# Kernel optimization log

Hardware: AMD Instinct MI355X
Metric: run time of the kernel (lower is better)

The kernel has to match this reference:

```python
import jax, jax.numpy as jnp
import numpy as np

N, S, D, d, H = 8, 2048, 256, 128, 10  # H = rel_k_heights
SCALING = float(np.sqrt(2 * d))


def _ln(x, g, b):
    m = jnp.mean(x, axis=-1, keepdims=True)
    v = jnp.var(x, axis=-1, keepdims=True)
    return (x - m) / jnp.sqrt(v + 1e-5) * g + b


def setup_inputs() -> dict:
    key = jax.random.key(0)
    ks = jax.random.split(key, 12)
    std = 0.02
    p = lambda k, shape: (jax.random.normal(k, shape, jnp.float32) * std)
    return {
        'sequence': jax.random.normal(ks[0], (N, S, D), jnp.float32),
        'attention_mask': jax.random.bernoulli(ks[1], 0.9, (N, S, S)),
        'heights': jax.random.randint(ks[2], (N, S), 0, 50),
        'W_init': p(ks[3], (D, D)), 'b_init': jnp.zeros((D,), jnp.float32),
        'ln_g': jnp.ones((D,), jnp.float32), 'ln_b': jnp.zeros((D,), jnp.float32),
        'W_U': p(ks[4], (D, 2 * D)), 'b_U': jnp.zeros((2 * D,), jnp.float32),
        'W_V': p(ks[5], (D, 2 * D)), 'b_V': jnp.zeros((2 * D,), jnp.float32),
        'W_Z': p(ks[6], (D, d)), 'b_Z': jnp.zeros((d,), jnp.float32),
        'os_gamma': p(ks[7], (3, d)),  # torch inits gamma ~ N(0, 0.02)
        'os_beta': jnp.zeros((3, d), jnp.float32),
        'embed_heights': jax.random.normal(ks[8], (H, d), jnp.float32),
        'W_out': p(ks[9], (2 * D, D)), 'b_out': jnp.zeros((D,), jnp.float32),
        'W_gate': p(ks[10], (2 * D, D)), 'b_gate': jnp.zeros((D,), jnp.float32),
    }


def reference(sequence, attention_mask, heights,
              W_init, b_init, ln_g, ln_b,
              W_U, b_U, W_V, b_V, W_Z, b_Z,
              os_gamma, os_beta, embed_heights,
              W_out, b_out, W_gate, b_gate):
    S0 = (S - 1) // 2  # 1023
    mask = attention_mask[:, :S0, S0:]          # [N,S0,S1]
    res = sequence

    x = _ln(sequence @ W_init + b_init, ln_g, ln_b)            # [N,S,D]
    U = jax.nn.silu(x[:, :S0, :] @ W_U + b_U)                  # [N,S0,2D]
    Z = jax.nn.silu(x @ W_Z + b_Z)                             # [N,S,d]
    V = jax.nn.silu(x[:, S0:, :] @ W_V + b_V)                  # [N,S1,2D]

    # OffsetScale: Q, Qp, K from Z
    Q = (Z * os_gamma[0] + os_beta[0])[:, :S0, :]              # [N,S0,d]
    Qp = (Z * os_gamma[1] + os_beta[1])[:, :S0, :]             # [N,S0,d]
    K = (Z * os_gamma[2] + os_beta[2])[:, S0:, :]              # [N,S1,d]

    energy = jnp.einsum('bsd,btd->bst', Q, K)                  # [N,S0,S1]

    # relative-height bias: direct gather (math-equivalent to one-hot*sum)
    Q_h = jnp.einsum('bsd,hd->bsh', Qp, embed_heights)         # [N,S0,H]
    rel = heights[:, None, S0:] - heights[:, :S0, None]        # [N,S0,S1]
    rel_idx = jnp.clip(rel, 1, H) - 1
    rel_energy = jnp.take_along_axis(Q_h, rel_idx, axis=2)     # [N,S0,S1]

    logits = (energy + rel_energy) / SCALING
    logits = jnp.where(mask, logits, -9999.0)
    attn = jax.nn.softmax(logits, axis=-1)                     # [N,S0,S1]

    V_ = jnp.einsum('bst,btd->bsd', attn, V)                   # [N,S0,2D]
    out = (U * V_) @ W_out + b_out                             # [N,S0,D]
    gates = jax.nn.sigmoid(
        jnp.concatenate([out, res[:, :S0, :]], axis=-1) @ W_gate + b_gate)
    out = gates * out + (1.0 - gates) * res[:, :S0, :]
    out = jnp.concatenate([out, res[:, S0:, :]], axis=1)       # [N,S,D]
    return out
```

## Files before the change

### kernel.cpp

```cpp
#include <hip/hip_runtime.h>
#include <cstdint>
#include <cstddef>

#define S_TOT 2048
#define S0_   1023
#define S1_   1025
#define D_    256
#define D2_   512
#define DZ_   128
#define NB_   8
#define NT_   17
#define KT16_ 68
#define SCALE_INV (1.0f/16.0f)
#define XPAD  264
#define UPAD  520
#define NTILES (NB_*S0_*NT_)
#define MP_BLOCKS ((NTILES + 15)/16)

typedef __attribute__((ext_vector_type(8))) short short8v;
typedef __attribute__((ext_vector_type(4))) short short4v;
typedef __attribute__((ext_vector_type(4))) float f32x4;
typedef unsigned long long u64;

__device__ __forceinline__ short f2bf(float f){
  unsigned u = __float_as_uint(f);
  unsigned r = (u + 0x7FFFu + ((u >> 16) & 1u)) >> 16;
  return (short)r;
}
__device__ __forceinline__ float bf2f(short s){
  return __uint_as_float(((unsigned)(unsigned short)s) << 16);
}
__device__ __forceinline__ float silu_f(float x){ return x / (1.f + __expf(-x)); }

__device__ __forceinline__ short8v load_afrag(const short* arow, int kt, int khi){
  short4v lo = *reinterpret_cast<const short4v*>(arow + kt*32 + khi);
  short4v hi = *reinterpret_cast<const short4v*>(arow + kt*32 + khi + 16);
  short8v r = {lo[0],lo[1],lo[2],lo[3],hi[0],hi[1],hi[2],hi[3]};
  return r;
}

__global__ __launch_bounds__(256) void k_prep(
    const float* __restrict__ W_init, const float* __restrict__ W_U,
    const float* __restrict__ W_V,    const float* __restrict__ W_Z,
    const float* __restrict__ W_out,  const float* __restrict__ W_gate,
    short* __restrict__ WpI, short* __restrict__ WpU, short* __restrict__ WpV,
    short* __restrict__ WpZ, short* __restrict__ WpO, short* __restrict__ WpG,
    const unsigned char* __restrict__ amask, u64* __restrict__ maskb)
{
  const int blk = blockIdx.x;
  if (blk < 304){
    const float* W; short* dst; int K, N, base;
    if      (blk <  32){ W=W_init; dst=WpI; K=256; N=256; base=0;   }
    else if (blk <  96){ W=W_U;    dst=WpU; K=256; N=512; base=32;  }
    else if (blk < 160){ W=W_V;    dst=WpV; K=256; N=512; base=96;  }
    else if (blk < 176){ W=W_Z;    dst=WpZ; K=256; N=128; base=160; }
    else if (blk < 240){ W=W_out;  dst=WpO; K=512; N=256; base=176; }
    else               { W=W_gate; dst=WpG; K=512; N=256; base=240; }
    const int wv = threadIdx.x >> 6, lane = threadIdx.x & 63;
    const int KT = K >> 5;
    const int tile = (blk - base)*4 + wv;
    const int nt = tile / KT, kt = tile - nt*KT;
    const int n = nt*16 + (lane & 15);
    const int kbase = kt*32 + ((lane>>4)<<2);
    short8v v;
    #pragma unroll
    for (int j=0;j<8;++j){
      int k = kbase + (j&3) + ((j>>2)<<4);
      v[j] = f2bf(W[(size_t)k*N + n]);
    }
    *reinterpret_cast<short8v*>(dst + ((size_t)tile*64 + lane)*8) = v;
  } else {
    const int lane = threadIdx.x & 63;
    const int g0 = ((blk - 304)*4 + (threadIdx.x >> 6))*4;
    #pragma unroll
    for (int j=0;j<4;++j){
      int tg = g0 + j;
      if (tg >= NTILES) break;
      int row = tg / NT_;
      int t   = tg - row*NT_;
      int b   = row / S0_;
      int q   = row - b*S0_;
      int key = t*64 + lane;
      unsigned char v = 0;
      if (key < S1_) v = amask[((size_t)(b*S_TOT + q))*S_TOT + S0_ + key];
      u64 bits = __ballot(v != 0);
      if (lane == 0) maskb[tg] = bits;
    }
  }
}

__global__ __launch_bounds__(256) void k_x(
    const float* __restrict__ seq, const short* __restrict__ Wp,
    const float* __restrict__ b_init,
    const float* __restrict__ ln_g, const float* __restrict__ ln_b,
    short* __restrict__ xb, float* __restrict__ out)
{
  __shared__ short s_a[64*XPAD];
  const int tid = threadIdx.x, lane = tid & 63, wv = tid >> 6;
  const int R0 = blockIdx.x * 64;
  const int colb = lane & 15, khi = (lane>>4)<<2;

  for (int c = tid; c < 64*64; c += 256){
    int row = c >> 6, c4 = (c & 63) << 2;
    int g = R0 + row;
    float4 f = *reinterpret_cast<const float4*>(seq + (size_t)g*D_ + c4);
    short4v h = { f2bf(f.x), f2bf(f.y), f2bf(f.z), f2bf(f.w) };
    *reinterpret_cast<short4v*>(&s_a[row*XPAD + c4]) = h;
    if ((g & 2047) >= S0_)
      *reinterpret_cast<float4*>(out + (size_t)g*D_ + c4) = f;
  }
  __syncthreads();

  f32x4 acc[16];
  #pragma unroll
  for (int nt=0;nt<16;++nt) acc[nt] = (f32x4){0.f,0.f,0.f,0.f};

  const short* arow = &s_a[(wv*16 + colb)*XPAD];
  #pragma unroll
  for (int kt=0; kt<8; ++kt){
    short8v a = load_afrag(arow, kt, khi);
    #pragma unroll
    for (int nt=0; nt<16; ++nt){
      short8v b = *reinterpret_cast<const short8v*>(Wp + ((size_t)(nt*8 + kt)*64 + lane)*8);
      acc[nt] = __builtin_amdgcn_mfma_f32_16x16x32_bf16(a, b, acc[nt], 0, 0, 0);
    }
  }

  float sum[4] = {0.f,0.f,0.f,0.f};
  #pragma unroll
  for (int nt=0; nt<16; ++nt){
    float bv = b_init[nt*16 + colb];
    #pragma unroll
    for (int r=0;r<4;++r){ acc[nt][r] += bv; sum[r] += acc[nt][r]; }
  }
  #pragma unroll
  for (int r=0;r<4;++r){
    #pragma unroll
    for (int m=1;m<16;m<<=1) sum[r] += __shfl_xor(sum[r], m, 64);
    sum[r] *= (1.f/256.f);
  }
  float var[4] = {0.f,0.f,0.f,0.f};
  #pragma unroll
  for (int nt=0; nt<16; ++nt)
    #pragma unroll
    for (int r=0;r<4;++r){ float d = acc[nt][r]-sum[r]; var[r] += d*d; }
  #pragma unroll
  for (int r=0;r<4;++r){
    #pragma unroll
    for (int m=1;m<16;m<<=1) var[r] += __shfl_xor(var[r], m, 64);
    var[r] = rsqrtf(var[r]*(1.f/256.f) + 1e-5f);
  }
  #pragma unroll
  for (int nt=0; nt<16; ++nt){
    int col = nt*16 + colb;
    float g = ln_g[col], bb = ln_b[col];
    #pragma unroll
    for (int r=0;r<4;++r){
      float xn = (acc[nt][r]-sum[r])*var[r]*g + bb;
      s_a[(wv*16 + ((lane>>4)<<2) + r)*XPAD + col] = f2bf(xn);
    }
  }
  __syncthreads();
  for (int c = tid; c < 64*32; c += 256){
    int row = c >> 5, c8 = (c & 31) << 3;
    *reinterpret_cast<short8v*>(xb + (size_t)(R0+row)*D_ + c8) =
        *reinterpret_cast<const short8v*>(&s_a[row*XPAD + c8]);
  }
}

__global__ __launch_bounds__(256) void k_gemmZV(
    const short* __restrict__ xb,
    const short* __restrict__ WpZ, const float* __restrict__ b_Z,
    short* __restrict__ Zb, short* __restrict__ ZkF,
    const short* __restrict__ WpV, const float* __restrict__ b_V,
    short* __restrict__ VtF)
{
  __shared__ short s_a[64*XPAD];
  __shared__ short s_t[64][72];
  const int blk = blockIdx.x;
  const int tid = threadIdx.x, lane = tid & 63, wv = tid >> 6;
  const int wy = wv >> 1, wx = wv & 1;
  const int colb = lane & 15, khi = (lane>>4)<<2;

  if (blk < 512){
    const int R0 = (blk >> 1) * 64;
    const int C0 = (blk & 1) * 64;

    for (int c = tid; c < 64*32; c += 256){
      int r = c >> 5, c8 = (c & 31) << 3;
      size_t xrow = (size_t)(R0 + r);
      *reinterpret_cast<short8v*>(&s_a[r*XPAD + c8]) =
          *reinterpret_cast<const short8v*>(xb + xrow*D_ + c8);
    }
    __syncthreads();

    f32x4 acc[2][2];
    #pragma unroll
    for(int i=0;i<2;++i)
      #pragma unroll
      for(int j=0;j<2;++j) acc[i][j] = (f32x4){0.f,0.f,0.f,0.f};

    const short* ar0 = &s_a[(wy*32 + colb)*XPAD];
    const short* ar1 = ar0 + 16*XPAD;
    const int ntg = (C0 >> 4) + wx*2;
    #pragma unroll
    for (int kt=0; kt<8; ++kt){
      short8v a0 = load_afrag(ar0, kt, khi);
      short8v a1 = load_afrag(ar1, kt, khi);
      short8v b0 = *reinterpret_cast<const short8v*>(WpZ + ((size_t)((ntg+0)*8 + kt)*64 + lane)*8);
      short8v b1 = *reinterpret_cast<const short8v*>(WpZ + ((size_t)((ntg+1)*8 + kt)*64 + lane)*8);
      acc[0][0] = __builtin_amdgcn_mfma_f32_16x16x32_bf16(a0, b0, acc[0][0], 0,0,0);
      acc[0][1] = __builtin_amdgcn_mfma_f32_16x16x32_bf16(a0, b1, acc[0][1], 0,0,0);
      acc[1][0] = __builtin_amdgcn_mfma_f32_16x16x32_bf16(a1, b0, acc[1][0], 0,0,0);
      acc[1][1] = __builtin_amdgcn_mfma_f32_16x16x32_bf16(a1, b1, acc[1][1], 0,0,0);
    }
    #pragma unroll
    for (int sj=0; sj<2; ++sj){
      int cl = wx*32 + sj*16 + colb;
      int col = C0 + cl;
      float bv = b_Z[col];
      #pragma unroll
      for (int si=0; si<2; ++si){
        #pragma unroll
        for (int r=0;r<4;++r){
          int rl = wy*32 + si*16 + ((lane>>4)<<2) + r;
          short zv = f2bf(silu_f(acc[si][sj][r] + bv));
          Zb[(size_t)(R0 + rl)*DZ_ + col] = zv;
          s_t[rl][cl] = zv;
        }
      }
    }
    __syncthreads();
    {
      const int r  = tid >> 2, hi = tid & 3;
      const int g  = R0 + r;
      const int s  = g & 2047;
      const int bb2= g >> 11;
      const int k  = s - S0_;
      if (k >= 0 && k <= 1024){
        const int kt16 = k >> 4, lcol = k & 15;
        const int lane2 = hi*16 + lcol;
        #pragma unroll
        for (int ktl=0; ktl<2; ++ktl){
          const int ktg = (C0 >> 5) + ktl;
          short8v f;
          #pragma unroll
          for (int j=0;j<8;++j){
            int dzl = ktl*32 + hi*4 + (j&3) + ((j>>2)<<4);
            f[j] = s_t[r][dzl];
          }
          size_t o = (((size_t)(bb2*KT16_ + kt16)*4 + ktg)*64 + lane2);
          *reinterpret_cast<short8v*>(ZkF + o*8) = f;
        }
      }
    }
  } else {
    const int idx = blk - 512;
    const int t   = idx % 17;
    const int rest= idx / 17;
    const int C0  = (rest & 7) * 64;
    const int b   = rest >> 3;
    const int R0  = t * 64;

    for (int c = tid; c < 64*32; c += 256){
      int r = c >> 5, c8 = (c & 31) << 3;
      int k = R0 + r; if (k > 1024) k = 1024;
      size_t xrow = (size_t)b*S_TOT + S0_ + k;
      *reinterpret_cast<short8v*>(&s_a[r*XPAD + c8]) =
          *reinterpret_cast<const short8v*>(xb + xrow*D_ + c8);
    }
    __syncthreads();

    f32x4 acc[2][2];
    #pragma unroll
    for(int i=0;i<2;++i)
      #pragma unroll
      for(int j=0;j<2;++j) acc[i][j] = (f32x4){0.f,0.f,0.f,0.f};

    const short* ar0 = &s_a[(wy*32 + colb)*XPAD];
    const short* ar1 = ar0 + 16*XPAD;
    const int ntg = (C0 >> 4) + wx*2;
    #pragma unroll
    for (int kt=0; kt<8; ++kt){
      short8v a0 = load_afrag(ar0, kt, khi);
      short8v a1 = load_afrag(ar1, kt, khi);
      short8v b0 = *reinterpret_cast<const short8v*>(WpV + ((size_t)((ntg+0)*8 + kt)*64 + lane)*8);
      short8v b1 = *reinterpret_cast<const short8v*>(WpV + ((size_t)((ntg+1)*8 + kt)*64 + lane)*8);
      acc[0][0] = __builtin_amdgcn_mfma_f32_16x16x32_bf16(a0, b0, acc[0][0], 0,0,0);
      acc[0][1] = __builtin_amdgcn_mfma_f32_16x16x32_bf16(a0, b1, acc[0][1], 0,0,0);
      acc[1][0] = __builtin_amdgcn_mfma_f32_16x16x32_bf16(a1, b0, acc[1][0], 0,0,0);
      acc[1][1] = __builtin_amdgcn_mfma_f32_16x16x32_bf16(a1, b1, acc[1][1], 0,0,0);
    }
    #pragma unroll
    for (int sj=0; sj<2; ++sj){
      int cl = wx*32 + sj*16 + colb;
      float bv = b_V[C0 + cl];
      #pragma unroll
      for (int si=0; si<2; ++si){
        #pragma unroll
        for (int r=0;r<4;++r){
          int rl = wy*32 + si*16 + ((lane>>4)<<2) + r;
          s_t[cl][rl] = f2bf(silu_f(acc[si][sj][r] + bv));
        }
      }
    }
    __syncthreads();
    {
      const int vt_l = tid >> 6;
      const int vloc = vt_l*16 + (lane & 15);
      const int krow = (lane>>4)<<2;
      #pragma unroll
      for (int kt=0; kt<2; ++kt){
        short8v f;
        #pragma unroll
        for (int j=0;j<8;++j){
          int kl = kt*32 + krow + (j&3) + ((j>>2)<<4);
          short v = s_t[vloc][kl];
          if (R0 + kl >= S1_) v = 0;
          f[j] = v;
        }
        size_t o = (((size_t)b*32 + (C0>>4) + vt_l)*(2*NT_) + 2*t + kt)*64 + lane;
        *reinterpret_cast<short8v*>(VtF + o*8) = f;
      }
    }
  }
}

#define SMEM_BYTES 103424
__global__ __launch_bounds__(512,2) void k_flash(
    const short* __restrict__ Zb, const short* __restrict__ ZkF,
    const short* __restrict__ VtF, const u64* __restrict__ maskb,
    const short* __restrict__ xb,
    const short* __restrict__ WpU, const float* __restrict__ b_U,
    const short* __restrict__ Wpo, const float* __restrict__ b_out,
    const short* __restrict__ Wpg, const float* __restrict__ b_gate,
    const float* __restrict__ seq, float* __restrict__ out,
    const int* __restrict__ heights,
    const float* __restrict__ os_g, const float* __restrict__ os_b,
    const float* __restrict__ embH)
{
  __shared__ __align__(16) char smem[SMEM_BYTES];
  __shared__ float  s_qh[32][12];
  __shared__ float  s_qb[32];
  __shared__ int    s_hk[NT_*64];
  __shared__ u64    s_mb[32][NT_];
  __shared__ float  s_mxA[8][16], s_mxB[8][16];
  __shared__ float  s_smA[8][16], s_smB[8][16];

  short8v (*s_pAl)[64] = reinterpret_cast<short8v(*)[64]>(smem);
  short8v (*s_pAh)[64] = reinterpret_cast<short8v(*)[64]>(smem + 17408);
  short8v (*s_pBl)[64] = reinterpret_cast<short8v(*)[64]>(smem + 34816);
  short8v (*s_pBh)[64] = reinterpret_cast<short8v(*)[64]>(smem + 52224);
  short   (*s_qg)[132] = reinterpret_cast<short(*)[132]>(smem + 34816);
  short* sUV = reinterpret_cast<short*>(smem);
  short* sO  = reinterpret_cast<short*>(smem + 34816);
  short* sX  = reinterpret_cast<short*>(smem + 69632);
  short* sR  = reinterpret_cast<short*>(smem + 86528);

  const int tid = threadIdx.x, lane = tid & 63, wv = tid >> 6;
  const int b  = blockIdx.x & 7;
  const int qp = blockIdx.x >> 3;
  const int q0 = qp * 32;

  for (int c = tid; c < 32*32; c += 512){
    int r = c >> 5, c8 = (c & 31) << 3;
    int q = min(q0 + r, S0_-1);
    *reinterpret_cast<short8v*>(&sX[r*XPAD + c8]) =
        *reinterpret_cast<const short8v*>(xb + ((size_t)(b*S_TOT + q))*D_ + c8);
  }
  for (int c = tid; c < 32*64; c += 512){
    int r = c >> 6, c4 = (c & 63) << 2;
    int q = min(q0 + r, S0_-1);
    float4 f = *reinterpret_cast<const float4*>(seq + ((size_t)(b*S_TOT + q))*D_ + c4);
    short4v h = { f2bf(f.x), f2bf(f.y), f2bf(f.z), f2bf(f.w) };
    *reinterpret_cast<short4v*>(&sR[r*XPAD + c4]) = h;
  }

  {
    int row = tid >> 4, part = tid & 15;
    int q = q0 + row; if (q > S0_-1) q = S0_-1;
    const short* zrow = Zb + ((size_t)(b*S_TOT + q))*DZ_ + part*8;
    float qb_acc = 0.f;
    float qh_acc[10];
    #pragma unroll
    for (int h=0;h<10;++h) qh_acc[h] = 0.f;
    #pragma unroll
    for (int e=0; e<8; ++e){
      int dz = part*8 + e;
      float z = bf2f(zrow[e]);
      float Q  = z*os_g[dz]      + os_b[dz];
      float Qp = z*os_g[DZ_+dz]  + os_b[DZ_+dz];
      s_qg[row][dz] = f2bf(Q * os_g[2*DZ_+dz]);
      qb_acc += Q * os_b[2*DZ_+dz];
      #pragma unroll
      for (int h=0;h<10;++h) qh_acc[h] += Qp * embH[h*DZ_ + dz];
    }
    #pragma unroll
    for (int m=1;m<16;m<<=1){
      qb_acc += __shfl_xor(qb_acc, m, 64);
      #pragma unroll
      for (int h=0;h<10;++h) qh_acc[h] += __shfl_xor(qh_acc[h], m, 64);
    }
    if (part == 0){
      s_qb[row] = qb_acc;
      #pragma unroll
      for (int h=0;h<10;++h) s_qh[row][h] = qh_acc[h];
    }
  }
  for (int k = tid; k < NT_*64; k += 512)
    s_hk[k] = (k < S1_) ? heights[b*S_TOT + S0_ + k] : 0;
  for (int idx = tid; idx < 32*NT_; idx += 512){
    int qq = idx / NT_, tt = idx - qq*NT_;
    int qr = min(q0 + qq, S0_-1);
    s_mb[qq][tt] = maskb[((size_t)(b*S0_ + qr))*NT_ + tt];
  }
  __syncthreads();

  const int qcol = lane & 15, khi = (lane>>4)<<2;
  const int hqA = heights[b*S_TOT + min(q0 + qcol,      S0_-1)];
  const int hqB = heights[b*S_TOT + min(q0 + 16 + qcol, S0_-1)];
  const float qbA = s_qb[qcol], qbB = s_qb[16 + qcol];

  short8v qgfA[4], qgfB[4];
  #pragma unroll
  for (int kt=0; kt<4; ++kt){
    qgfA[kt] = load_afrag(&s_qg[qcol][0],      kt, khi);
    qgfB[kt] = load_afrag(&s_qg[16 + qcol][0], kt, khi);
  }

  f32x4 scA[3][4], scB[3][4];
  float tmA = -1e30f, tmB = -1e30f;
  #pragma unroll
  for (int it=0; it<3; ++it){
    const int t = it*8 + wv;
    if (t < NT_){
      u64 mbA = s_mb[qcol][t], mbB = s_mb[16 + qcol][t];
      #pragma unroll
      for (int st=0; st<4; ++st){
        f32x4 cA = (f32x4){0.f,0.f,0.f,0.f};
        f32x4 cB = (f32x4){0.f,0.f,0.f,0.f};
        #pragma unroll
        for (int kt=0; kt<4; ++kt){
          short8v a = *reinterpret_cast<const short8v*>(
              ZkF + (((size_t)(b*KT16_ + t*4 + st)*4 + kt)*64 + lane)*8);
          cA = __builtin_amdgcn_mfma_f32_16x16x32_bf16(a, qgfA[kt], cA, 0,0,0);
          cB = __builtin_amdgcn_mfma_f32_16x16x32_bf16(a, qgfB[kt], cB, 0,0,0);
        }
        int4 hk4 = *reinterpret_cast<const int4*>(&s_hk[t*64 + st*16 + khi]);
        #pragma unroll
        for (int r=0;r<4;++r){
          int hk = (&hk4.x)[r];
          int kl = st*16 + khi + r;
          int iA = min(max(hk - hqA, 1), 10) - 1;
          float vA = (cA[r] + qbA + s_qh[qcol][iA]) * SCALE_INV;
          vA = ((mbA >> kl) & 1ull) ? vA : -9999.f;
          cA[r] = vA; tmA = fmaxf(tmA, vA);
          int iB = min(max(hk - hqB, 1), 10) - 1;
          float vB = (cB[r] + qbB + s_qh[16 + qcol][iB]) * SCALE_INV;
          vB = ((mbB >> kl) & 1ull) ? vB : -9999.f;
          cB[r] = vB; tmB = fmaxf(tmB, vB);
        }
        scA[it][st] = cA; scB[it][st] = cB;
      }
    }
  }
  tmA = fmaxf(tmA, __shfl_xor(tmA, 16, 64));
  tmA = fmaxf(tmA, __shfl_xor(tmA, 32, 64));
  tmB = fmaxf(tmB, __shfl_xor(tmB, 16, 64));
  tmB = fmaxf(tmB, __shfl_xor(tmB, 32, 64));
  if (lane < 16){ s_mxA[wv][lane] = tmA; s_mxB[wv][lane] = tmB; }
  __syncthreads();

  float mA = -1e30f, mB = -1e30f;
  #pragma unroll
  for (int w=0; w<8; ++w){
    mA = fmaxf(mA, s_mxA[w][qcol]);
    mB = fmaxf(mB, s_mxB[w][qcol]);
  }
  float lsA = 0.f, lsB = 0.f;
  #pragma unroll
  for (int it=0; it<3; ++it){
    const int t = it*8 + wv;
    if (t < NT_){
      #pragma unroll
      for (int st=0; st<4; ++st)
        #pragma unroll
        for (int r=0;r<4;++r){
          float pA = __expf(scA[it][st][r] - mA); lsA += pA; scA[it][st][r] = pA;
          float pB = __expf(scB[it][st][r] - mB); lsB += pB; scB[it][st][r] = pB;
        }
      short8v a0, a1, b0, b1;
      #pragma unroll
      for (int j=0;j<8;++j){
        a0[j] = f2bf(scA[it][(j>>2)][j&3]);
        a1[j] = f2bf(scA[it][2 + (j>>2)][j&3]);
        b0[j] = f2bf(scB[it][(j>>2)][j&3]);
        b1[j] = f2bf(scB[it][2 + (j>>2)][j&3]);
      }
      s_pAl[t][lane] = a0; s_pAh[t][lane] = a1;
      s_pBl[t][lane] = b0; s_pBh[t][lane] = b1;
    }
  }
  lsA += __shfl_xor(lsA, 16, 64); lsA += __shfl_xor(lsA, 32, 64);
  lsB += __shfl_xor(lsB, 16, 64); lsB += __shfl_xor(lsB, 32, 64);
  if (lane < 16){ s_smA[wv][lane] = lsA; s_smB[wv][lane] = lsB; }
  __syncthreads();

  float lrA[4], lrB[4];
  #pragma unroll
  for (int r=0;r<4;++r){
    int qr = khi + r;
    float sa = 0.f, sb = 0.f;
    #pragma unroll
    for (int w=0; w<8; ++w){ sa += s_smA[w][qr]; sb += s_smB[w][qr]; }
    lrA[r] = sa; lrB[r] = sb;
  }
  f32x4 OA[4], OB[4];
  #pragma unroll
  for (int j=0;j<4;++j){ OA[j] = (f32x4){0.f,0.f,0.f,0.f}; OB[j] = (f32x4){0.f,0.f,0.f,0.f}; }
  for (int t=0; t<NT_; ++t){
    short8v pa0 = s_pAl[t][lane], pa1 = s_pAh[t][lane];
    short8v pb0 = s_pBl[t][lane], pb1 = s_pBh[t][lane];
    #pragma unroll
    for (int j=0;j<4;++j){
      size_t vb = ((size_t)b*32 + wv*4 + j)*(2*NT_) + 2*t;
      short8v v0 = *reinterpret_cast<const short8v*>(VtF + (vb*64 + lane)*8);
      short8v v1 = *reinterpret_cast<const short8v*>(VtF + ((vb+1)*64 + lane)*8);
      OA[j] = __builtin_amdgcn_mfma_f32_16x16x32_bf16(pa0, v0, OA[j], 0,0,0);
      OA[j] = __builtin_amdgcn_mfma_f32_16x16x32_bf16(pa1, v1, OA[j], 0,0,0);
      OB[j] = __builtin_amdgcn_mfma_f32_16x16x32_bf16(pb0, v0, OB[j], 0,0,0);
      OB[j] = __builtin_amdgcn_mfma_f32_16x16x32_bf16(pb1, v1, OB[j], 0,0,0);
    }
  }
  __syncthreads();

  f32x4 auA[4], auB[4];
  #pragma unroll
  for (int j=0;j<4;++j){ auA[j] = (f32x4){0.f,0.f,0.f,0.f}; auB[j] = (f32x4){0.f,0.f,0.f,0.f}; }
  {
    const short* xrA = &sX[qcol*XPAD];
    const short* xrB = &sX[(16 + qcol)*XPAD];
    #pragma unroll
    for (int kt=0; kt<8; ++kt){
      short8v aA = load_afrag(xrA, kt, khi);
      short8v aB = load_afrag(xrB, kt, khi);
      #pragma unroll
      for (int j=0;j<4;++j){
        int nt = wv*4 + j;
        short8v bw = *reinterpret_cast<const short8v*>(WpU + ((size_t)(nt*8 + kt)*64 + lane)*8);
        auA[j] = __builtin_amdgcn_mfma_f32_16x16x32_bf16(aA, bw, auA[j], 0,0,0);
        auB[j] = __builtin_amdgcn_mfma_f32_16x16x32_bf16(aB, bw, auB[j], 0,0,0);
      }
    }
  }
  float invA[4], invB[4];
  #pragma unroll
  for (int r=0;r<4;++r){ invA[r] = 1.f / lrA[r]; invB[r] = 1.f / lrB[r]; }
  #pragma unroll
  for (int j=0;j<4;++j){
    int v = wv*64 + j*16 + qcol;
    float bu = b_U[v];
    #pragma unroll
    for (int r=0;r<4;++r){
      float uA = silu_f(auA[j][r] + bu);
      sUV[(khi + r)*UPAD + v] = f2bf(uA * OA[j][r] * invA[r]);
      float uB = silu_f(auB[j][r] + bu);
      sUV[(16 + khi + r)*UPAD + v] = f2bf(uB * OB[j][r] * invB[r]);
    }
  }
  __syncthreads();

  f32x4 aoA[2], aoB[2];
  #pragma unroll
  for (int j=0;j<2;++j){ aoA[j] = (f32x4){0.f,0.f,0.f,0.f}; aoB[j] = (f32x4){0.f,0.f,0.f,0.f}; }
  {
    const short* uvA = &sUV[qcol*UPAD];
    const short* uvB = &sUV[(16 + qcol)*UPAD];
    #pragma unroll
    for (int kt=0; kt<16; ++kt){
      short8v aA = load_afrag(uvA, kt, khi);
      short8v aB = load_afrag(uvB, kt, khi);
      #pragma unroll
      for (int j=0;j<2;++j){
        int nt = wv*2 + j;
        short8v bw = *reinterpret_cast<const short8v*>(Wpo + ((size_t)(nt*16 + kt)*64 + lane)*8);
        aoA[j] = __builtin_amdgcn_mfma_f32_16x16x32_bf16(aA, bw, aoA[j], 0,0,0);
        aoB[j] = __builtin_amdgcn_mfma_f32_16x16x32_bf16(aB, bw, aoB[j], 0,0,0);
      }
    }
  }
  #pragma unroll
  for (int j=0;j<2;++j){
    int col = (wv*2+j)*16 + qcol;
    float bv = b_out[col];
    #pragma unroll
    for (int r=0;r<4;++r){
      aoA[j][r] += bv;  sO[(khi + r)*XPAD + col]      = f2bf(aoA[j][r]);
      aoB[j][r] += bv;  sO[(16 + khi + r)*XPAD + col] = f2bf(aoB[j][r]);
    }
  }
  __syncthreads();

  f32x4 agA[2], agB[2];
  #pragma unroll
  for (int j=0;j<2;++j){ agA[j] = (f32x4){0.f,0.f,0.f,0.f}; agB[j] = (f32x4){0.f,0.f,0.f,0.f}; }
  {
    const short* oA = &sO[qcol*XPAD];
    const short* oB = &sO[(16 + qcol)*XPAD];
    const short* rA = &sR[qcol*XPAD];
    const short* rB = &sR[(16 + qcol)*XPAD];
    #pragma unroll
    for (int kt=0; kt<8; ++kt){
      short8v aA = load_afrag(oA, kt, khi);
      short8v aB = load_afrag(oB, kt, khi);
      #pragma unroll
      for (int j=0;j<2;++j){
        int nt = wv*2 + j;
        short8v bw = *reinterpret_cast<const short8v*>(Wpg + ((size_t)(nt*16 + kt)*64 + lane)*8);
        agA[j] = __builtin_amdgcn_mfma_f32_16x16x32_bf16(aA, bw, agA[j], 0,0,0);
        agB[j] = __builtin_amdgcn_mfma_f32_16x16x32_bf16(aB, bw, agB[j], 0,0,0);
      }
    }
    #pragma unroll
    for (int kt=0; kt<8; ++kt){
      short8v aA = load_afrag(rA, kt, khi);
      short8v aB = load_afrag(rB, kt, khi);
      #pragma unroll
      for (int j=0;j<2;++j){
        int nt = wv*2 + j;
        short8v bw = *reinterpret_cast<const short8v*>(Wpg + ((size_t)(nt*16 + 8 + kt)*64 + lane)*8);
        agA[j] = __builtin_amdgcn_mfma_f32_16x16x32_bf16(aA, bw, agA[j], 0,0,0);
        agB[j] = __builtin_amdgcn_mfma_f32_16x16x32_bf16(aB, bw, agB[j], 0,0,0);
      }
    }
  }
  #pragma unroll
  for (int j=0;j<2;++j){
    int col = (wv*2+j)*16 + qcol;
    float bg = b_gate[col];
    #pragma unroll
    for (int r=0;r<4;++r){
      int qA = q0 + khi + r;
      if (qA < S0_){
        float res = seq[((size_t)(b*S_TOT + qA))*D_ + col];
        float g = 1.f/(1.f + __expf(-(agA[j][r] + bg)));
        out[((size_t)(b*S_TOT + qA))*D_ + col] = g*aoA[j][r] + (1.f-g)*res;
      }
      int qB = q0 + 16 + khi + r;
      if (qB < S0_){
        float res = seq[((size_t)(b*S_TOT + qB))*D_ + col];
        float g = 1.f/(1.f + __expf(-(agB[j][r] + bg)));
        out[((size_t)(b*S_TOT + qB))*D_ + col] = g*aoB[j][r] + (1.f-g)*res;
      }
    }
  }
}

extern "C" void kernel_launch(void* const* d_in, const int* in_sizes, int n_in,
                              void* d_out, int out_size, void* d_ws, size_t ws_size,
                              hipStream_t stream)
{
  const float* seq    = (const float*)d_in[0];
  const unsigned char* amask = (const unsigned char*)d_in[1];
  const int*   heights= (const int*)d_in[2];
  const float* W_init = (const float*)d_in[3];
  const float* b_init = (const float*)d_in[4];
  const float* ln_g   = (const float*)d_in[5];
  const float* ln_b   = (const float*)d_in[6];
  const float* W_U    = (const float*)d_in[7];
  const float* b_U    = (const float*)d_in[8];
  const float* W_V    = (const float*)d_in[9];
  const float* b_V    = (const float*)d_in[10];
  const float* W_Z    = (const float*)d_in[11];
  const float* b_Z    = (const float*)d_in[12];
  const float* os_g   = (const float*)d_in[13];
  const float* os_b   = (const float*)d_in[14];
  const float* embH   = (const float*)d_in[15];
  const float* W_out  = (const float*)d_in[16];
  const float* b_out  = (const float*)d_in[17];
  const float* W_gate = (const float*)d_in[18];
  const float* b_gate = (const float*)d_in[19];
  float* out = (float*)d_out;

  char* w = (char*)d_ws;
  short* Zb  = (short*)w;                w += (size_t)16512*128*2;
  short* VtF = (short*)w;                w += (size_t)8*32*(2*NT_)*64*8*2;
  short* ZkF = (short*)w;                w += (size_t)NB_*KT16_*4*64*8*2;
  short* xb  = (short*)w;                w += (size_t)16384*256*2;
  u64*  maskb = (u64*)w;                 w += (size_t)NB_*S0_*NT_*8;
  short* WpI = (short*)w;                w += (size_t)65536*2;
  short* WpU = (short*)w;                w += (size_t)131072*2;
  short* WpV = (short*)w;                w += (size_t)131072*2;
  short* WpZ = (short*)w;                w += (size_t)32768*2;
  short* WpO = (short*)w;                w += (size_t)131072*2;
  short* WpG = (short*)w;                w += (size_t)131072*2;

  hipLaunchKernelGGL(k_prep, dim3(304 + MP_BLOCKS), dim3(256), 0, stream,
      W_init, W_U, W_V, W_Z, W_out, W_gate,
      WpI, WpU, WpV, WpZ, WpO, WpG, amask, maskb);

  hipLaunchKernelGGL(k_x, dim3(256), dim3(256), 0, stream,
      seq, WpI, b_init, ln_g, ln_b, xb, out);

  hipLaunchKernelGGL(k_gemmZV, dim3(512 + 1088), dim3(256), 0, stream,
      xb, WpZ, b_Z, Zb, ZkF, WpV, b_V, VtF);

  hipLaunchKernelGGL(k_flash, dim3(256), dim3(512), 0, stream,
      Zb, ZkF, VtF, maskb, xb, WpU, b_U, WpO, b_out, WpG, b_gate,
      seq, out, heights, os_g, os_b, embH);
}
```

Baseline: 95.47 us.

## Cut LDS and register footprint of flash kernel to raise occupancy

Shrinks the fused attention kernel's shared memory by merging the x and residual staging buffers into one region loaded later, and by storing key heights as shorts. The score computation for the two 16-row query halves is split into sequential passes, which halves live score registers. Launch bounds move from 2 to 4 blocks per CU to exploit this. The trade-off is that the Zk fragments are loaded twice from global memory and there are extra barriers.

```diff
diff --git a/kernel.cpp b/kernel.cpp
--- a/kernel.cpp
+++ b/kernel.cpp
@@ -326,8 +326,8 @@
   }
 }
 
-#define SMEM_BYTES 103424
-__global__ __launch_bounds__(512,2) void k_flash(
+#define SMEM_BYTES 69632
+__global__ __launch_bounds__(512,4) void k_flash(
     const short* __restrict__ Zb, const short* __restrict__ ZkF,
     const short* __restrict__ VtF, const u64* __restrict__ maskb,
     const short* __restrict__ xb,
@@ -342,7 +342,7 @@
   __shared__ __align__(16) char smem[SMEM_BYTES];
   __shared__ float  s_qh[32][12];
   __shared__ float  s_qb[32];
-  __shared__ int    s_hk[NT_*64];
+  __shared__ short  s_hk[NT_*64];
   __shared__ u64    s_mb[32][NT_];
   __shared__ float  s_mxA[8][16], s_mxB[8][16];
   __shared__ float  s_smA[8][16], s_smB[8][16];
@@ -353,28 +353,13 @@
   short8v (*s_pBh)[64] = reinterpret_cast<short8v(*)[64]>(smem + 52224);
   short   (*s_qg)[132] = reinterpret_cast<short(*)[132]>(smem + 34816);
   short* sUV = reinterpret_cast<short*>(smem);
-  short* sO  = reinterpret_cast<short*>(smem + 34816);
-  short* sX  = reinterpret_cast<short*>(smem + 69632);
-  short* sR  = reinterpret_cast<short*>(smem + 86528);
+  short* sO  = reinterpret_cast<short*>(smem + 33280);
+  short* sXR = reinterpret_cast<short*>(smem + 50176);
 
   const int tid = threadIdx.x, lane = tid & 63, wv = tid >> 6;
   const int b  = blockIdx.x & 7;
   const int qp = blockIdx.x >> 3;
   const int q0 = qp * 32;
-
-  for (int c = tid; c < 32*32; c += 512){
-    int r = c >> 5, c8 = (c & 31) << 3;
-    int q = min(q0 + r, S0_-1);
-    *reinterpret_cast<short8v*>(&sX[r*XPAD + c8]) =
-        *reinterpret_cast<const short8v*>(xb + ((size_t)(b*S_TOT + q))*D_ + c8);
-  }
-  for (int c = tid; c < 32*64; c += 512){
-    int r = c >> 6, c4 = (c & 63) << 2;
-    int q = min(q0 + r, S0_-1);
-    float4 f = *reinterpret_cast<const float4*>(seq + ((size_t)(b*S_TOT + q))*D_ + c4);
-    short4v h = { f2bf(f.x), f2bf(f.y), f2bf(f.z), f2bf(f.w) };
-    *reinterpret_cast<short4v*>(&sR[r*XPAD + c4]) = h;
-  }
 
   {
     int row = tid >> 4, part = tid & 15;
@@ -408,7 +393,7 @@
     }
   }
   for (int k = tid; k < NT_*64; k += 512)
-    s_hk[k] = (k < S1_) ? heights[b*S_TOT + S0_ + k] : 0;
+    s_hk[k] = (k < S1_) ? (short)heights[b*S_TOT + S0_ + k] : (short)0;
   for (int idx = tid; idx < 32*NT_; idx += 512){
     int qq = idx / NT_, tt = idx - qq*NT_;
     int qr = min(q0 + qq, S0_-1);
@@ -427,83 +412,133 @@
     qgfA[kt] = load_afrag(&s_qg[qcol][0],      kt, khi);
     qgfB[kt] = load_afrag(&s_qg[16 + qcol][0], kt, khi);
   }
-
-  f32x4 scA[3][4], scB[3][4];
-  float tmA = -1e30f, tmB = -1e30f;
+  __syncthreads();
+
+  const short* zkb = ZkF + (size_t)b*KT16_*4*512;
+
+  f32x4 scA[3][4];
+  float tmA = -1e30f;
   #pragma unroll
   for (int it=0; it<3; ++it){
     const int t = it*8 + wv;
     if (t < NT_){
-      u64 mbA = s_mb[qcol][t], mbB = s_mb[16 + qcol][t];
+      u64 mbA = s_mb[qcol][t];
       #pragma unroll
       for (int st=0; st<4; ++st){
         f32x4 cA = (f32x4){0.f,0.f,0.f,0.f};
-        f32x4 cB = (f32x4){0.f,0.f,0.f,0.f};
         #pragma unroll
         for (int kt=0; kt<4; ++kt){
-          short8v a = *reinterpret_cast<const short8v*>(
-              ZkF + (((size_t)(b*KT16_ + t*4 + st)*4 + kt)*64 + lane)*8);
+          short8v a = *reinterpret_cast<const short8v*>(zkb + ((t*16 + st*4 + kt)*64 + lane)*8);
           cA = __builtin_amdgcn_mfma_f32_16x16x32_bf16(a, qgfA[kt], cA, 0,0,0);
-          cB = __builtin_amdgcn_mfma_f32_16x16x32_bf16(a, qgfB[kt], cB, 0,0,0);
-        }
-        int4 hk4 = *reinterpret_cast<const int4*>(&s_hk[t*64 + st*16 + khi]);
+        }
+        short4v hk4 = *reinterpret_cast<const short4v*>(&s_hk[t*64 + st*16 + khi]);
         #pragma unroll
         for (int r=0;r<4;++r){
-          int hk = (&hk4.x)[r];
+          int hk = (int)hk4[r];
           int kl = st*16 + khi + r;
           int iA = min(max(hk - hqA, 1), 10) - 1;
           float vA = (cA[r] + qbA + s_qh[qcol][iA]) * SCALE_INV;
           vA = ((mbA >> kl) & 1ull) ? vA : -9999.f;
           cA[r] = vA; tmA = fmaxf(tmA, vA);
+        }
+        scA[it][st] = cA;
+      }
+    }
+  }
+  tmA = fmaxf(tmA, __shfl_xor(tmA, 16, 64));
+  tmA = fmaxf(tmA, __shfl_xor(tmA, 32, 64));
+  if (lane < 16) s_mxA[wv][lane] = tmA;
+  __syncthreads();
+
+  {
+    float mA = -1e30f;
+    #pragma unroll
+    for (int w=0; w<8; ++w) mA = fmaxf(mA, s_mxA[w][qcol]);
+    float lsA = 0.f;
+    #pragma unroll
+    for (int it=0; it<3; ++it){
+      const int t = it*8 + wv;
+      if (t < NT_){
+        #pragma unroll
+        for (int st=0; st<4; ++st)
+          #pragma unroll
+          for (int r=0;r<4;++r){
+            float pA = __expf(scA[it][st][r] - mA); lsA += pA; scA[it][st][r] = pA;
+          }
+        short8v a0, a1;
+        #pragma unroll
+        for (int j=0;j<8;++j){
+          a0[j] = f2bf(scA[it][(j>>2)][j&3]);
+          a1[j] = f2bf(scA[it][2 + (j>>2)][j&3]);
+        }
+        s_pAl[t][lane] = a0; s_pAh[t][lane] = a1;
+      }
+    }
+    lsA += __shfl_xor(lsA, 16, 64); lsA += __shfl_xor(lsA, 32, 64);
+    if (lane < 16) s_smA[wv][lane] = lsA;
+  }
+
+  f32x4 scB[3][4];
+  float tmB = -1e30f;
+  #pragma unroll
+  for (int it=0; it<3; ++it){
+    const int t = it*8 + wv;
+    if (t < NT_){
+      u64 mbB = s_mb[16 + qcol][t];
+      #pragma unroll
+      for (int st=0; st<4; ++st){
+        f32x4 cB = (f32x4){0.f,0.f,0.f,0.f};
+        #pragma unroll
+        for (int kt=0; kt<4; ++kt){
+          short8v a = *reinterpret_cast<const short8v*>(zkb + ((t*16 + st*4 + kt)*64 + lane)*8);
+          cB = __builtin_amdgcn_mfma_f32_16x16x32_bf16(a, qgfB[kt], cB, 0,0,0);
+        }
+        short4v hk4 = *reinterpret_cast<const short4v*>(&s_hk[t*64 + st*16 + khi]);
+        #pragma unroll
+        for (int r=0;r<4;++r){
+          int hk = (int)hk4[r];
+          int kl = st*16 + khi + r;
           int iB = min(max(hk - hqB, 1), 10) - 1;
           float vB = (cB[r] + qbB + s_qh[16 + qcol][iB]) * SCALE_INV;
           vB = ((mbB >> kl) & 1ull) ? vB : -9999.f;
           cB[r] = vB; tmB = fmaxf(tmB, vB);
         }
-        scA[it][st] = cA; scB[it][st] = cB;
-      }
-    }
-  }
-  tmA = fmaxf(tmA, __shfl_xor(tmA, 16, 64));
-  tmA = fmaxf(tmA, __shfl_xor(tmA, 32, 64));
+        scB[it][st] = cB;
+      }
+    }
+  }
   tmB = fmaxf(tmB, __shfl_xor(tmB, 16, 64));
   tmB = fmaxf(tmB, __shfl_xor(tmB, 32, 64));
-  if (lane < 16){ s_mxA[wv][lane] = tmA; s_mxB[wv][lane] = tmB; }
-  __syncthreads();
-
-  float mA = -1e30f, mB = -1e30f;
-  #pragma unroll
-  for (int w=0; w<8; ++w){
-    mA = fmaxf(mA, s_mxA[w][qcol]);
-    mB = fmaxf(mB, s_mxB[w][qcol]);
-  }
-  float lsA = 0.f, lsB = 0.f;
-  #pragma unroll
-  for (int it=0; it<3; ++it){
-    const int t = it*8 + wv;
-    if (t < NT_){
-      #pragma unroll
-      for (int st=0; st<4; ++st)
-        #pragma unroll
-        for (int r=0;r<4;++r){
-          float pA = __expf(scA[it][st][r] - mA); lsA += pA; scA[it][st][r] = pA;
-          float pB = __expf(scB[it][st][r] - mB); lsB += pB; scB[it][st][r] = pB;
-        }
-      short8v a0, a1, b0, b1;
-      #pragma unroll
-      for (int j=0;j<8;++j){
-        a0[j] = f2bf(scA[it][(j>>2)][j&3]);
-        a1[j] = f2bf(scA[it][2 + (j>>2)][j&3]);
-        b0[j] = f2bf(scB[it][(j>>2)][j&3]);
-        b1[j] = f2bf(scB[it][2 + (j>>2)][j&3]);
-      }
-      s_pAl[t][lane] = a0; s_pAh[t][lane] = a1;
-      s_pBl[t][lane] = b0; s_pBh[t][lane] = b1;
-    }
-  }
-  lsA += __shfl_xor(lsA, 16, 64); lsA += __shfl_xor(lsA, 32, 64);
-  lsB += __shfl_xor(lsB, 16, 64); lsB += __shfl_xor(lsB, 32, 64);
-  if (lane < 16){ s_smA[wv][lane] = lsA; s_smB[wv][lane] = lsB; }
+  if (lane < 16) s_mxB[wv][lane] = tmB;
+  __syncthreads();
+
+  {
+    float mB = -1e30f;
+    #pragma unroll
+    for (int w=0; w<8; ++w) mB = fmaxf(mB, s_mxB[w][qcol]);
+    float lsB = 0.f;
+    #pragma unroll
+    for (int it=0; it<3; ++it){
+      const int t = it*8 + wv;
+      if (t < NT_){
+        #pragma unroll
+        for (int st=0; st<4; ++st)
+          #pragma unroll
+          for (int r=0;r<4;++r){
+            float pB = __expf(scB[it][st][r] - mB); lsB += pB; scB[it][st][r] = pB;
+          }
+        short8v b0, b1;
+        #pragma unroll
+        for (int j=0;j<8;++j){
+          b0[j] = f2bf(scB[it][(j>>2)][j&3]);
+          b1[j] = f2bf(scB[it][2 + (j>>2)][j&3]);
+        }
+        s_pBl[t][lane] = b0; s_pBh[t][lane] = b1;
+      }
+    }
+    lsB += __shfl_xor(lsB, 16, 64); lsB += __shfl_xor(lsB, 32, 64);
+    if (lane < 16) s_smB[wv][lane] = lsB;
+  }
   __syncthreads();
 
   float lrA[4], lrB[4];
@@ -534,12 +569,20 @@
   }
   __syncthreads();
 
+  for (int c = tid; c < 32*32; c += 512){
+    int r = c >> 5, c8 = (c & 31) << 3;
+    int q = min(q0 + r, S0_-1);
+    *reinterpret_cast<short8v*>(&sXR[r*XPAD + c8]) =
+        *reinterpret_cast<const short8v*>(xb + ((size_t)(b*S_TOT + q))*D_ + c8);
+  }
+  __syncthreads();
+
   f32x4 auA[4], auB[4];
   #pragma unroll
   for (int j=0;j<4;++j){ auA[j] = (f32x4){0.f,0.f,0.f,0.f}; auB[j] = (f32x4){0.f,0.f,0.f,0.f}; }
   {
-    const short* xrA = &sX[qcol*XPAD];
-    const short* xrB = &sX[(16 + qcol)*XPAD];
+    const short* xrA = &sXR[qcol*XPAD];
+    const short* xrB = &sXR[(16 + qcol)*XPAD];
     #pragma unroll
     for (int kt=0; kt<8; ++kt){
       short8v aA = load_afrag(xrA, kt, khi);
@@ -570,6 +613,14 @@
   }
   __syncthreads();
 
+  for (int c = tid; c < 32*64; c += 512){
+    int r = c >> 6, c4 = (c & 63) << 2;
+    int q = min(q0 + r, S0_-1);
+    float4 f = *reinterpret_cast<const float4*>(seq + ((size_t)(b*S_TOT + q))*D_ + c4);
+    short4v h = { f2bf(f.x), f2bf(f.y), f2bf(f.z), f2bf(f.w) };
+    *reinterpret_cast<short4v*>(&sXR[r*XPAD + c4]) = h;
+  }
+
   f32x4 aoA[2], aoB[2];
   #pragma unroll
   for (int j=0;j<2;++j){ aoA[j] = (f32x4){0.f,0.f,0.f,0.f}; aoB[j] = (f32x4){0.f,0.f,0.f,0.f}; }
@@ -607,8 +658,8 @@
   {
     const short* oA = &sO[qcol*XPAD];
     const short* oB = &sO[(16 + qcol)*XPAD];
-    const short* rA = &sR[qcol*XPAD];
-    const short* rB = &sR[(16 + qcol)*XPAD];
+    const short* rA = &sXR[qcol*XPAD];
+    const short* rB = &sXR[(16 + qcol)*XPAD];
     #pragma unroll
     for (int kt=0; kt<8; ++kt){
       short8v aA = load_afrag(oA, kt, khi);
```

New measurement: 124.6 us. +30.5%, slower.
